# Optimization experiments

Measured on AMD Instinct MI355X. Metric: run time of the kernel, lower is better.

## Reference

```python
import jax, jax.numpy as jnp
import numpy as np

INPUT_SIZE = 1024
ATTN_SIZE = 1024


def setup_inputs() -> dict:
    key = jax.random.key(0)
    ks = jax.random.split(key, 7)
    s = 1.0 / np.sqrt(INPUT_SIZE)
    x = jax.random.normal(ks[0], (2048, 8, INPUT_SIZE), dtype=jnp.float32)
    Wq = jax.random.uniform(ks[1], (ATTN_SIZE, INPUT_SIZE), jnp.float32, -s, s)
    bq = jax.random.uniform(ks[2], (ATTN_SIZE,), jnp.float32, -s, s)
    Wk = jax.random.uniform(ks[3], (ATTN_SIZE, INPUT_SIZE), jnp.float32, -s, s)
    bk = jax.random.uniform(ks[4], (ATTN_SIZE,), jnp.float32, -s, s)
    Wv = jax.random.uniform(ks[5], (ATTN_SIZE, INPUT_SIZE), jnp.float32, -s, s)
    bv = jax.random.uniform(ks[6], (ATTN_SIZE,), jnp.float32, -s, s)
    return {"x": x, "Wq": Wq, "bq": bq, "Wk": Wk, "bk": bk, "Wv": Wv, "bv": bv}


def reference(x, Wq, bq, Wk, bk, Wv, bv):
    # x: (S, B, D) -> (B, S, D)
    xb = jnp.swapaxes(x, 0, 1)
    Q = jnp.einsum('bsd,ad->bsa', xb, Wq) + bq  # (B, S, A)
    K = jnp.einsum('bsd,ad->bsa', xb, Wk) + bk
    V = jnp.einsum('bsd,ad->bsa', xb, Wv) + bv
    S = Q.shape[1]
    scores = jnp.einsum('bqa,bka->bqk', Q, K) / jnp.sqrt(jnp.float32(ATTN_SIZE))
    causal = jnp.tril(jnp.ones((S, S), dtype=bool))  # True where attended
    scores = jnp.where(causal, scores, -jnp.inf)
    probs = jax.nn.softmax(scores, axis=-1)
    out = jnp.einsum('bqk,bka->bqa', probs, V)  # (B, S, A)
    return jnp.swapaxes(out, 0, 1)  # (S, B, A)
```

## Files before the change

### kernel.cpp

```cpp
#include <hip/hip_runtime.h>
#include <hip/hip_bf16.h>
#include <math.h>

typedef short bf16x8 __attribute__((ext_vector_type(8)));
typedef float f32x4 __attribute__((ext_vector_type(4)));
typedef short short4v __attribute__((ext_vector_type(4)));
typedef short short8v __attribute__((ext_vector_type(8)));

__device__ __forceinline__ short f2bf(float f) {
  unsigned u = __builtin_bit_cast(unsigned, f);
  unsigned r = (u + 0x7FFFu + ((u >> 16) & 1u)) >> 16;
  return (short)r;
}
__device__ __forceinline__ float bf2f(short s) {
  unsigned u = ((unsigned)(unsigned short)s) << 16;
  return __builtin_bit_cast(float, u);
}

typedef __attribute__((address_space(1))) const unsigned g_u32;
typedef __attribute__((address_space(3))) unsigned l_u32;
__device__ __forceinline__ void gload_lds16(const short* g, short* l) {
  __builtin_amdgcn_global_load_lds((g_u32*)g, (l_u32*)l, 16, 0, 0);
}


__global__ __launch_bounds__(256) void k_cast_x(const float* __restrict__ x, short* __restrict__ xb) {
  int tid = blockIdx.x * 256 + threadIdx.x;
  int d4 = tid & 255;
  int sb = tid >> 8;
  int s = sb & 2047;
  int b = sb >> 11;
  float4 v = *((const float4*)(x + (((size_t)s * 8 + b) << 10)) + d4);
  short4v o;
  o.x = f2bf(v.x); o.y = f2bf(v.y); o.z = f2bf(v.z); o.w = f2bf(v.w);
  *((short4v*)(xb + (((size_t)b * 2048 + s) << 10)) + d4) = o;
}

__global__ __launch_bounds__(256) void k_cast_w(const float* __restrict__ Wq, const float* __restrict__ Wk,
                                                const float* __restrict__ Wv, short* __restrict__ Wcat) {
  int tid = blockIdx.x * 256 + threadIdx.x;
  int d4 = tid & 255;
  int n = tid >> 8;
  const float* src = (n < 1024) ? Wq : (n < 2048 ? Wk : Wv);
  int nl = n & 1023;
  float4 v = *((const float4*)(src + ((size_t)nl << 10)) + d4);
  short4v o;
  o.x = f2bf(v.x); o.y = f2bf(v.y); o.z = f2bf(v.z); o.w = f2bf(v.w);
  *((short4v*)(Wcat + ((size_t)n << 10)) + d4) = o;
}

__global__ __launch_bounds__(256) void k_cast_bias(const float* __restrict__ bq, const float* __restrict__ bk,
                                                   const float* __restrict__ bv, float* __restrict__ biascat) {
  int i = blockIdx.x * 256 + threadIdx.x;
  if (i < 3072) biascat[i] = (i < 1024) ? bq[i] : (i < 2048 ? bk[i & 1023] : bv[i & 1023]);
}

template <int LDA, int LDB>
__device__ __forceinline__ void gemm256_core(const short* __restrict__ Ag, const short* __restrict__ Bg,
                                             int NT, short* __restrict__ lds, f32x4 (&acc)[8][4], int tid) {
  const int lane = tid & 63;
  const int wid = tid >> 6;
  const int wm = wid >> 2, wn = wid & 3;
  const int r15 = lane & 15;
  const int g = lane >> 4;
  const int co = ((g ^ ((r15 >> 1) & 3)) << 3);
  short* As = lds;
  short* Bs = lds + 32768;

  auto stage_pair = [&](int bufv, int kkv, int kElem) {
    short* Al = As + (bufv * 2 + kkv) * 8192;
    short* Bl = Bs + (bufv * 2 + kkv) * 8192;
#pragma unroll
    for (int i = 0; i < 2; ++i) {
      int c = i * 512 + tid;
      int r = c >> 2, s = c & 3;
      int gk = kElem + ((s ^ ((r >> 1) & 3)) << 3);
      gload_lds16(Ag + (size_t)r * LDA + gk, Al + c * 8);
    }
#pragma unroll
    for (int i = 0; i < 2; ++i) {
      int c = i * 512 + tid;
      int r = c >> 2, s = c & 3;
      int gk = kElem + ((s ^ ((r >> 1) & 3)) << 3);
      gload_lds16(Bg + (size_t)r * LDB + gk, Bl + c * 8);
    }
  };

  bf16x8 af[8], b0, b1;
  auto lda = [&](int bufv, int kk) {
    const short* Ab = As + ((bufv * 2 + kk) * 256 + wm * 128 + r15) * 32 + co;
#pragma unroll
    for (int mi = 0; mi < 8; ++mi) af[mi] = *(const bf16x8*)(Ab + mi * 512);
  };
  auto ldb = [&](int bufv, int kk, int nh) {
    const short* Bb = Bs + ((bufv * 2 + kk) * 256 + wn * 64 + nh * 32 + r15) * 32 + co;
    b0 = *(const bf16x8*)(Bb);
    b1 = *(const bf16x8*)(Bb + 512);
  };
  auto fire = [&](int nh) {
    __builtin_amdgcn_s_barrier();
    asm volatile("s_waitcnt lgkmcnt(0)" ::: "memory");
    __builtin_amdgcn_sched_barrier(0);
    __builtin_amdgcn_s_setprio(1);
#pragma unroll
    for (int mi = 0; mi < 8; ++mi) {
      acc[mi][nh * 2 + 0] = __builtin_amdgcn_mfma_f32_16x16x32_bf16(af[mi], b0, acc[mi][nh * 2 + 0], 0, 0, 0);
      acc[mi][nh * 2 + 1] = __builtin_amdgcn_mfma_f32_16x16x32_bf16(af[mi], b1, acc[mi][nh * 2 + 1], 0, 0, 0);
    }
    __builtin_amdgcn_s_setprio(0);
  };

  stage_pair(0, 0, 0);
  stage_pair(0, 1, 32);
  stage_pair(1, 0, 64);
  asm volatile("s_waitcnt vmcnt(8)" ::: "memory");
  __builtin_amdgcn_s_barrier();

  for (int t = 0; t < NT - 2; ++t) {
    const int buf = t & 1, nbuf = buf ^ 1;
    lda(buf, 0); ldb(buf, 0, 0); stage_pair(nbuf, 1, ((t + 1) << 6) + 32);
    fire(0);
    __builtin_amdgcn_s_barrier();
    ldb(buf, 0, 1);
    fire(1);
    asm volatile("s_waitcnt vmcnt(8)" ::: "memory");
    __builtin_amdgcn_s_barrier();
    lda(buf, 1); ldb(buf, 1, 0); stage_pair(buf, 0, (t + 2) << 6);
    fire(0);
    __builtin_amdgcn_s_barrier();
    ldb(buf, 1, 1);
    fire(1);
    asm volatile("s_waitcnt vmcnt(8)" ::: "memory");
    __builtin_amdgcn_s_barrier();
  }
  {
    const int t = NT - 2, buf = t & 1, nbuf = buf ^ 1;
    lda(buf, 0); ldb(buf, 0, 0); stage_pair(nbuf, 1, ((t + 1) << 6) + 32);
    fire(0);
    __builtin_amdgcn_s_barrier();
    ldb(buf, 0, 1);
    fire(1);
    asm volatile("s_waitcnt vmcnt(8)" ::: "memory");
    __builtin_amdgcn_s_barrier();
    lda(buf, 1); ldb(buf, 1, 0);
    fire(0);
    __builtin_amdgcn_s_barrier();
    ldb(buf, 1, 1);
    fire(1);
    asm volatile("s_waitcnt vmcnt(4)" ::: "memory");
    __builtin_amdgcn_s_barrier();
  }
  {
    const int buf = (NT - 1) & 1;
    lda(buf, 0); ldb(buf, 0, 0);
    fire(0);
    __builtin_amdgcn_s_barrier();
    ldb(buf, 0, 1);
    fire(1);
    asm volatile("s_waitcnt vmcnt(0)" ::: "memory");
    __builtin_amdgcn_s_barrier();
    lda(buf, 1); ldb(buf, 1, 0);
    fire(0);
    __builtin_amdgcn_s_barrier();
    ldb(buf, 1, 1);
    fire(1);
    __builtin_amdgcn_s_barrier();
  }
}

__global__ __launch_bounds__(512, 1) void k_proj(const short* __restrict__ Xb, const short* __restrict__ Wc,
                                                 const float* __restrict__ biascat,
                                                 short* __restrict__ Q, short* __restrict__ K, short* __restrict__ Vt) {
  __shared__ __align__(16) short lds[65536];
  int tid = threadIdx.x;
  int wg = blockIdx.x;
  int swz = (wg & 7) * 96 + (wg >> 3);
  int mt = swz / 12, nt = swz % 12;
  int m0 = mt << 8, n0 = nt << 8;
  f32x4 acc[8][4] = {};
  gemm256_core<1024, 1024>(Xb + (size_t)m0 * 1024, Wc + (size_t)n0 * 1024, 16, lds, acc, tid);
  int lane = tid & 63, wid = tid >> 6;
  int wm = wid >> 2, wn = wid & 3;
  int r15 = lane & 15;
  int which = n0 >> 10;
  int nbase = n0 & 1023;
  if (which == 2) {
#pragma unroll
    for (int ni = 0; ni < 4; ++ni) {
      int cth = wn * 64 + ni * 16 + r15;
      int a = nbase + cth;
      float bv = biascat[n0 + cth];
#pragma unroll
      for (int mi = 0; mi < 8; ++mi) {
        int r = m0 + wm * 128 + mi * 16 + ((lane >> 4) << 2);
        int b = r >> 11, s = r & 2047;
        short4v o;
#pragma unroll
        for (int j = 0; j < 4; ++j) o[j] = f2bf(acc[mi][ni][j] + bv);
        *(short4v*)(Vt + ((size_t)b << 21) + ((size_t)a << 11) + s) = o;
      }
    }
  } else {
    short* outb = (which == 0) ? Q : K;
#pragma unroll
    for (int ni = 0; ni < 4; ++ni) {
      int cth = wn * 64 + ni * 16 + r15;
      float bv = biascat[n0 + cth];
#pragma unroll
      for (int mi = 0; mi < 8; ++mi)
#pragma unroll
        for (int j = 0; j < 4; ++j) {
          int r = m0 + wm * 128 + mi * 16 + ((lane >> 4) << 2) + j;
          outb[((size_t)r << 10) + nbase + cth] = f2bf(acc[mi][ni][j] + bv);
        }
    }
  }
}

__global__ __launch_bounds__(512, 1) void k_qk(const short* __restrict__ Q, const short* __restrict__ K,
                                               short* __restrict__ Sc) {
  int nt = blockIdx.x, mt = blockIdx.y, b = blockIdx.z;
  if (nt > mt) return;
  __shared__ __align__(16) short lds[65536];
  int tid = threadIdx.x;
  int m0 = mt << 8, n0 = nt << 8;
  const short* Qb = Q + ((size_t)b << 21);
  const short* Kb = K + ((size_t)b << 21);
  f32x4 acc[8][4] = {};
  gemm256_core<1024, 1024>(Qb + (size_t)m0 * 1024, Kb + (size_t)n0 * 1024, 16, lds, acc, tid);
  short* Sb = Sc + ((size_t)b << 22);
  int lane = tid & 63, wid = tid >> 6;
  int wm = wid >> 2, wn = wid & 3;
  int r15 = lane & 15;
#pragma unroll
  for (int mi = 0; mi < 8; ++mi)
#pragma unroll
    for (int ni = 0; ni < 4; ++ni)
#pragma unroll
      for (int j = 0; j < 4; ++j) {
        int r = m0 + wm * 128 + mi * 16 + ((lane >> 4) << 2) + j;
        int c = n0 + wn * 64 + ni * 16 + r15;
        Sb[((size_t)r << 11) + c] = f2bf(acc[mi][ni][j] * 0.03125f);
      }
}

__global__ __launch_bounds__(256) void k_softmax(short* __restrict__ Sc) {
  int row = blockIdx.x;
  int b = row >> 11, q = row & 2047;
  short* Pr = Sc + ((size_t)b << 22) + ((size_t)q << 11);
  int T = ((q >> 8) + 1) << 8;
  int tid = threadIdx.x, lane = tid & 63, wid = tid >> 6;
  int k0 = tid << 3;
  float v[8];
  if (k0 < T) {
    short8v raw = *(const short8v*)(Pr + k0);
#pragma unroll
    for (int j = 0; j < 8; ++j) v[j] = (k0 + j <= q) ? bf2f(raw[j]) : -__builtin_inff();
  } else {
#pragma unroll
    for (int j = 0; j < 8; ++j) v[j] = -__builtin_inff();
  }
  float mx = v[0];
#pragma unroll
  for (int j = 1; j < 8; ++j) mx = fmaxf(mx, v[j]);
  for (int off = 1; off < 64; off <<= 1) mx = fmaxf(mx, __shfl_xor(mx, off, 64));
  __shared__ float red[2][4];
  if (lane == 0) red[0][wid] = mx;
  __syncthreads();
  mx = fmaxf(fmaxf(red[0][0], red[0][1]), fmaxf(red[0][2], red[0][3]));
  float e[8], sum = 0.f;
#pragma unroll
  for (int j = 0; j < 8; ++j) {
    e[j] = exp2f((v[j] - mx) * 1.4426950408889634f);
    sum += e[j];
  }
  for (int off = 1; off < 64; off <<= 1) sum += __shfl_xor(sum, off, 64);
  if (lane == 0) red[1][wid] = sum;
  __syncthreads();
  sum = red[1][0] + red[1][1] + red[1][2] + red[1][3];
  float inv = 1.f / sum;
  if (k0 < T) {
    short8v o;
#pragma unroll
    for (int j = 0; j < 8; ++j) o[j] = (k0 + j <= q) ? f2bf(e[j] * inv) : (short)0;
    *(short8v*)(Pr + k0) = o;
  }
}

__global__ __launch_bounds__(512, 1) void k_pv(const short* __restrict__ P, const short* __restrict__ Vt,
                                               float* __restrict__ out) {
  int nt = blockIdx.x, mt = blockIdx.y, b = blockIdx.z;
  __shared__ __align__(16) short lds[65536];
  int tid = threadIdx.x;
  int m0 = mt << 8, n0 = nt << 8;
  const short* Pb = P + ((size_t)b << 22);
  const short* Vtb = Vt + ((size_t)b << 21);
  f32x4 acc[8][4] = {};
  gemm256_core<2048, 2048>(Pb + (size_t)m0 * 2048, Vtb + (size_t)n0 * 2048, 4 * (mt + 1), lds, acc, tid);
  int lane = tid & 63, wid = tid >> 6;
  int wm = wid >> 2, wn = wid & 3;
  int r15 = lane & 15;
#pragma unroll
  for (int mi = 0; mi < 8; ++mi)
#pragma unroll
    for (int ni = 0; ni < 4; ++ni)
#pragma unroll
      for (int j = 0; j < 4; ++j) {
        int r = m0 + wm * 128 + mi * 16 + ((lane >> 4) << 2) + j;
        int c = n0 + wn * 64 + ni * 16 + r15;
        out[((size_t)r << 13) + ((size_t)b << 10) + c] = acc[mi][ni][j];
      }
}

extern "C" void kernel_launch(void* const* d_in, const int* in_sizes, int n_in,
                              void* d_out, int out_size, void* d_ws, size_t ws_size,
                              hipStream_t stream) {
  const float* x  = (const float*)d_in[0];
  const float* Wq = (const float*)d_in[1];
  const float* bq = (const float*)d_in[2];
  const float* Wk = (const float*)d_in[3];
  const float* bk = (const float*)d_in[4];
  const float* Wv = (const float*)d_in[5];
  const float* bv = (const float*)d_in[6];
  float* out = (float*)d_out;
  char* ws = (char*)d_ws;

  short* xb   = (short*)(ws);
  short* Wcat = (short*)(ws + 33554432);
  float* bias = (float*)(ws + 39845888);
  short* Q    = (short*)(ws + 39858176);
  short* K    = (short*)(ws + 73412608);
  short* Vt   = (short*)(ws + 106967040);
  short* Sc   = (short*)(ws + 140521472);

  k_cast_x<<<16384, 256, 0, stream>>>(x, xb);
  k_cast_w<<<3072, 256, 0, stream>>>(Wq, Wk, Wv, Wcat);
  k_cast_bias<<<12, 256, 0, stream>>>(bq, bk, bv, bias);
  k_proj<<<768, 512, 0, stream>>>(xb, Wcat, bias, Q, K, Vt);
  k_qk<<<dim3(8, 8, 8), 512, 0, stream>>>(Q, K, Sc);
  k_softmax<<<16384, 256, 0, stream>>>(Sc);
  k_pv<<<dim3(4, 8, 8), 512, 0, stream>>>(Sc, Vt, out);
}
```

Before: 292.7 us.

## Simplify GEMM mainloop to whole-tile double buffering with fewer barriers

Replaces the fine-grained half-K-step staging schedule of the 256x256 GEMM core, which used many barriers and interleaved fire phases, with a simpler loop. Each iteration prefetches the whole next K=64 tile into the other buffer, waits once, and then runs all 32 MFMAs per K-half from fragments loaded up front. This cuts barrier count and per-phase LDS wait stalls. In exchange it loses finer overlap of global loads with compute and holds more B fragments in registers at once.

Result: slower. 325.0 us (+11.0%).

```diff
diff --git a/kernel.cpp b/kernel.cpp
--- a/kernel.cpp
+++ b/kernel.cpp
@@ -67,104 +67,75 @@
   short* As = lds;
   short* Bs = lds + 32768;
 
-  auto stage_pair = [&](int bufv, int kkv, int kElem) {
-    short* Al = As + (bufv * 2 + kkv) * 8192;
-    short* Bl = Bs + (bufv * 2 + kkv) * 8192;
-#pragma unroll
-    for (int i = 0; i < 2; ++i) {
-      int c = i * 512 + tid;
-      int r = c >> 2, s = c & 3;
-      int gk = kElem + ((s ^ ((r >> 1) & 3)) << 3);
-      gload_lds16(Ag + (size_t)r * LDA + gk, Al + c * 8);
-    }
-#pragma unroll
-    for (int i = 0; i < 2; ++i) {
-      int c = i * 512 + tid;
-      int r = c >> 2, s = c & 3;
-      int gk = kElem + ((s ^ ((r >> 1) & 3)) << 3);
-      gload_lds16(Bg + (size_t)r * LDB + gk, Bl + c * 8);
+  auto stage_tile = [&](int bufv, int kElem) {
+#pragma unroll
+    for (int kkv = 0; kkv < 2; ++kkv) {
+      short* Al = As + (bufv * 2 + kkv) * 8192;
+      short* Bl = Bs + (bufv * 2 + kkv) * 8192;
+      int ke = kElem + kkv * 32;
+#pragma unroll
+      for (int i = 0; i < 2; ++i) {
+        int c = i * 512 + tid;
+        int r = c >> 2, s = c & 3;
+        int gk = ke + ((s ^ ((r >> 1) & 3)) << 3);
+        gload_lds16(Ag + (size_t)r * LDA + gk, Al + c * 8);
+      }
+#pragma unroll
+      for (int i = 0; i < 2; ++i) {
+        int c = i * 512 + tid;
+        int r = c >> 2, s = c & 3;
+        int gk = ke + ((s ^ ((r >> 1) & 3)) << 3);
+        gload_lds16(Bg + (size_t)r * LDB + gk, Bl + c * 8);
+      }
     }
   };
 
-  bf16x8 af[8], b0, b1;
-  auto lda = [&](int bufv, int kk) {
-    const short* Ab = As + ((bufv * 2 + kk) * 256 + wm * 128 + r15) * 32 + co;
-#pragma unroll
-    for (int mi = 0; mi < 8; ++mi) af[mi] = *(const bf16x8*)(Ab + mi * 512);
-  };
-  auto ldb = [&](int bufv, int kk, int nh) {
-    const short* Bb = Bs + ((bufv * 2 + kk) * 256 + wn * 64 + nh * 32 + r15) * 32 + co;
-    b0 = *(const bf16x8*)(Bb);
-    b1 = *(const bf16x8*)(Bb + 512);
-  };
-  auto fire = [&](int nh) {
+  stage_tile(0, 0);
+
+  for (int t = 0; t < NT; ++t) {
+    const int buf = t & 1;
     __builtin_amdgcn_s_barrier();
-    asm volatile("s_waitcnt lgkmcnt(0)" ::: "memory");
-    __builtin_amdgcn_sched_barrier(0);
-    __builtin_amdgcn_s_setprio(1);
-#pragma unroll
-    for (int mi = 0; mi < 8; ++mi) {
-      acc[mi][nh * 2 + 0] = __builtin_amdgcn_mfma_f32_16x16x32_bf16(af[mi], b0, acc[mi][nh * 2 + 0], 0, 0, 0);
-      acc[mi][nh * 2 + 1] = __builtin_amdgcn_mfma_f32_16x16x32_bf16(af[mi], b1, acc[mi][nh * 2 + 1], 0, 0, 0);
-    }
-    __builtin_amdgcn_s_setprio(0);
-  };
-
-  stage_pair(0, 0, 0);
-  stage_pair(0, 1, 32);
-  stage_pair(1, 0, 64);
-  asm volatile("s_waitcnt vmcnt(8)" ::: "memory");
-  __builtin_amdgcn_s_barrier();
-
-  for (int t = 0; t < NT - 2; ++t) {
-    const int buf = t & 1, nbuf = buf ^ 1;
-    lda(buf, 0); ldb(buf, 0, 0); stage_pair(nbuf, 1, ((t + 1) << 6) + 32);
-    fire(0);
+    if (t + 1 < NT) {
+      stage_tile(buf ^ 1, (t + 1) << 6);
+      asm volatile("s_waitcnt vmcnt(8)" ::: "memory");
+    } else {
+      asm volatile("s_waitcnt vmcnt(0)" ::: "memory");
+    }
     __builtin_amdgcn_s_barrier();
-    ldb(buf, 0, 1);
-    fire(1);
-    asm volatile("s_waitcnt vmcnt(8)" ::: "memory");
-    __builtin_amdgcn_s_barrier();
-    lda(buf, 1); ldb(buf, 1, 0); stage_pair(buf, 0, (t + 2) << 6);
-    fire(0);
-    __builtin_amdgcn_s_barrier();
-    ldb(buf, 1, 1);
-    fire(1);
-    asm volatile("s_waitcnt vmcnt(8)" ::: "memory");
-    __builtin_amdgcn_s_barrier();
-  }
-  {
-    const int t = NT - 2, buf = t & 1, nbuf = buf ^ 1;
-    lda(buf, 0); ldb(buf, 0, 0); stage_pair(nbuf, 1, ((t + 1) << 6) + 32);
-    fire(0);
-    __builtin_amdgcn_s_barrier();
-    ldb(buf, 0, 1);
-    fire(1);
-    asm volatile("s_waitcnt vmcnt(8)" ::: "memory");
-    __builtin_amdgcn_s_barrier();
-    lda(buf, 1); ldb(buf, 1, 0);
-    fire(0);
-    __builtin_amdgcn_s_barrier();
-    ldb(buf, 1, 1);
-    fire(1);
-    asm volatile("s_waitcnt vmcnt(4)" ::: "memory");
-    __builtin_amdgcn_s_barrier();
-  }
-  {
-    const int buf = (NT - 1) & 1;
-    lda(buf, 0); ldb(buf, 0, 0);
-    fire(0);
-    __builtin_amdgcn_s_barrier();
-    ldb(buf, 0, 1);
-    fire(1);
-    asm volatile("s_waitcnt vmcnt(0)" ::: "memory");
-    __builtin_amdgcn_s_barrier();
-    lda(buf, 1); ldb(buf, 1, 0);
-    fire(0);
-    __builtin_amdgcn_s_barrier();
-    ldb(buf, 1, 1);
-    fire(1);
-    __builtin_amdgcn_s_barrier();
+
+    const short* A0 = As + ((buf * 2 + 0) * 256 + wm * 128 + r15) * 32 + co;
+    const short* B0 = Bs + ((buf * 2 + 0) * 256 + wn * 64 + r15) * 32 + co;
+    const short* A1 = As + ((buf * 2 + 1) * 256 + wm * 128 + r15) * 32 + co;
+    const short* B1 = Bs + ((buf * 2 + 1) * 256 + wn * 64 + r15) * 32 + co;
+
+    {
+      bf16x8 af[8], bfr[4];
+#pragma unroll
+      for (int mi = 0; mi < 8; ++mi) af[mi] = *(const bf16x8*)(A0 + mi * 512);
+#pragma unroll
+      for (int ni = 0; ni < 4; ++ni) bfr[ni] = *(const bf16x8*)(B0 + ni * 512);
+      __builtin_amdgcn_s_setprio(1);
+#pragma unroll
+      for (int mi = 0; mi < 8; ++mi)
+#pragma unroll
+        for (int ni = 0; ni < 4; ++ni)
+          acc[mi][ni] = __builtin_amdgcn_mfma_f32_16x16x32_bf16(af[mi], bfr[ni], acc[mi][ni], 0, 0, 0);
+      __builtin_amdgcn_s_setprio(0);
+    }
+    {
+      bf16x8 af[8], bfr[4];
+#pragma unroll
+      for (int mi = 0; mi < 8; ++mi) af[mi] = *(const bf16x8*)(A1 + mi * 512);
+#pragma unroll
+      for (int ni = 0; ni < 4; ++ni) bfr[ni] = *(const bf16x8*)(B1 + ni * 512);
+      __builtin_amdgcn_s_setprio(1);
+#pragma unroll
+      for (int mi = 0; mi < 8; ++mi)
+#pragma unroll
+        for (int ni = 0; ni < 4; ++ni)
+          acc[mi][ni] = __builtin_amdgcn_mfma_f32_16x16x32_bf16(af[mi], bfr[ni], acc[mi][ni], 0, 0, 0);
+      __builtin_amdgcn_s_setprio(0);
+    }
   }
 }
 
```
